# Kernel optimization log

Hardware: AMD Instinct MI355X
Metric: run time of the kernel (lower is better)

## Reference

```python
import jax, jax.numpy as jnp
import numpy as np

N, D, L = 524288, 64, 20  # tokens, in_features, chain depth (20 Linear layers per branch)


def setup_inputs() -> dict:
    key = jax.random.key(0)
    kx, kw, kb = jax.random.split(key, 3)
    x = jax.random.normal(kx, (N, D), dtype=jnp.float32)
    # torch.nn.Linear default init: U(-1/sqrt(fan_in), 1/sqrt(fan_in))
    bound = 1.0 / np.sqrt(D)
    W = jax.random.uniform(kw, (L, D, D), dtype=jnp.float32, minval=-bound, maxval=bound)
    b = jax.random.uniform(kb, (L, D), dtype=jnp.float32, minval=-bound, maxval=bound)
    return {"x": x, "W": W, "b": b}


def reference(x, W, b):
    # is_hit=False => scatter routes ALL tokens to path 1 (path 0 is empty),
    # so forward = branches[1]: 20 sequential Linear(D, D) layers, then a
    # trivial gather (concat of the single non-empty branch result).
    # torch Linear: y = x @ W^T + b, W has shape [out, in].
    def step(h, wb):
        w, bias = wb  # w: [D, D], bias: [D]
        return h @ w.T + bias, None

    out, _ = jax.lax.scan(step, x, (W, b))
    return out
```

## Files before the change

### kernel.cpp

```cpp
#include <hip/hip_runtime.h>
#include <stdint.h>


using short8  = __attribute__((ext_vector_type(8))) short;
using floatx4 = __attribute__((ext_vector_type(4))) float;

#define N_TOK   524288
#define N_LAYER 20
#define FPERM(mt, m) (32 * ((mt) >> 1) + 8 * ((m) >> 2) + 4 * ((mt) & 1) + ((m) & 3))

#ifdef __has_builtin
#if __has_builtin(__builtin_amdgcn_cvt_pk_bf16_f32)
#define HAVE_CVT_PK_BF16 1
#endif
#endif

#ifdef HAVE_CVT_PK_BF16
typedef __bf16 bf16x2_t __attribute__((ext_vector_type(2)));
__device__ __forceinline__ uint32_t pk_bf16(float lo, float hi) {
  union { bf16x2_t v; uint32_t u; } c;
  c.v = __builtin_amdgcn_cvt_pk_bf16_f32(lo, hi);
  return c.u;
}
#else
__device__ __forceinline__ uint32_t pk_bf16(float lo, float hi) {
  uint32_t a = __float_as_uint(lo) + 0x8000u;
  uint32_t b = __float_as_uint(hi) + 0x8000u;
  return __builtin_amdgcn_perm(b, a, 0x07060302u);
}
#endif

__device__ __forceinline__ float upk_lo(uint32_t p) { return __uint_as_float(p << 16); }
__device__ __forceinline__ float upk_hi(uint32_t p) { return __uint_as_float(p & 0xffff0000u); }

__device__ __forceinline__ uint16_t bf16_rne(float f) {
  uint32_t u = __float_as_uint(f);
  u += 0x7fffu + ((u >> 16) & 1u);
  return (uint16_t)(u >> 16);
}
__device__ __forceinline__ float bf16_dec(uint16_t h) {
  return __uint_as_float(((uint32_t)h) << 16);
}

union BFrag { short8 v; uint32_t u[4]; uint4 raw; };
union AFrag { short8 v; uint32_t u[4]; uint4 raw; };

__global__ void prep_split(const float* __restrict__ W,
                           uint16_t* __restrict__ wsh, uint16_t* __restrict__ wsl) {
  int idx  = blockIdx.x * 256 + threadIdx.x;
  int l    = idx >> 9;
  int rem  = idx & 511;
  int frag = rem >> 6;
  int lane = rem & 63;
  int mt = frag >> 1, ks = frag & 1;
  int m  = lane & 15;
  int q  = lane >> 4;
  int wrow = FPERM(mt, m);
  const float* src = W + l * 4096 + wrow * 64 + 32 * ks + 8 * q;
  float4 f0 = *(const float4*)(src);
  float4 f1 = *(const float4*)(src + 4);
  float w[8] = {f0.x, f0.y, f0.z, f0.w, f1.x, f1.y, f1.z, f1.w};
  union { uint16_t s[8]; uint4 v; } oh, ol;
  #pragma unroll
  for (int j = 0; j < 8; j++) {
    uint16_t h = bf16_rne(w[j]);
    oh.s[j] = h;
    ol.s[j] = bf16_rne(w[j] - bf16_dec(h));
  }
  *(uint4*)(wsh + (size_t)idx * 8) = oh.v;
  *(uint4*)(wsl + (size_t)idx * 8) = ol.v;
}

__global__ __launch_bounds__(128, 1) void compose(
    const uint16_t* __restrict__ wsh, const uint16_t* __restrict__ wsl,
    const float* __restrict__ bias,
    uint16_t* __restrict__ afrag, float* __restrict__ vout)
{
  __shared__ float comp[65][64];
  __shared__ __align__(16) float biasLds[N_LAYER * 64];

  const int tid  = threadIdx.x;
  const int twv  = tid >> 6;
  const int lane = tid & 63;
  const int tl   = lane & 15;
  const int q    = lane >> 4;

  for (int i = tid; i < N_LAYER * 64; i += 128) biasLds[i] = bias[i];

  BFrag Bh[4][2], Bl[4][2];
  #pragma unroll
  for (int tb = 0; tb < 4; tb++) {
    const int tok = twv * 64 + tb * 16 + tl;
    #pragma unroll
    for (int ks = 0; ks < 2; ks++)
      #pragma unroll
      for (int p = 0; p < 4; p++) {
        const int f0 = 32 * ks + 8 * q + 2 * p;
        Bh[tb][ks].u[p] = pk_bf16(tok == f0 ? 1.0f : 0.0f, tok == f0 + 1 ? 1.0f : 0.0f);
        Bl[tb][ks].u[p] = 0u;
      }
  }

  const uint4* wph = (const uint4*)wsh;
  const uint4* wpl = (const uint4*)wsl;

  AFrag Ah[8], Al[8];
  #pragma unroll
  for (int f = 0; f < 8; f++) {
    Ah[f].raw = wph[f * 64 + lane];
    Al[f].raw = wpl[f * 64 + lane];
  }

  __syncthreads();

  floatx4 acc[4][4];
  #pragma unroll 2
  for (int l = 0; l < N_LAYER; l++) {
    const int ln = (l + 1 < N_LAYER) ? l + 1 : N_LAYER - 1;
    uint4 nh[8], nl[8];
    #pragma unroll
    for (int f = 0; f < 8; f++) {
      nh[f] = wph[(ln * 8 + f) * 64 + lane];
      nl[f] = wpl[(ln * 8 + f) * 64 + lane];
    }

    #pragma unroll
    for (int mt = 0; mt < 4; mt++) {
      floatx4 bv = *(const floatx4*)(biasLds + l * 64 + 32 * (mt >> 1) + 4 * (mt & 1) + 8 * q);
      #pragma unroll
      for (int tb = 0; tb < 4; tb++) acc[tb][mt] = bv;
    }

    #pragma unroll
    for (int ks = 0; ks < 2; ks++)
      #pragma unroll
      for (int mt = 0; mt < 4; mt++) {
        const int f = mt * 2 + ks;
        #pragma unroll
        for (int tb = 0; tb < 4; tb++) {
          acc[tb][mt] = __builtin_amdgcn_mfma_f32_16x16x32_bf16(Ah[f].v, Bh[tb][ks].v, acc[tb][mt], 0, 0, 0);
          acc[tb][mt] = __builtin_amdgcn_mfma_f32_16x16x32_bf16(Ah[f].v, Bl[tb][ks].v, acc[tb][mt], 0, 0, 0);
          acc[tb][mt] = __builtin_amdgcn_mfma_f32_16x16x32_bf16(Al[f].v, Bh[tb][ks].v, acc[tb][mt], 0, 0, 0);
        }
      }

    if (l == N_LAYER - 1) break;

    #pragma unroll
    for (int tb = 0; tb < 4; tb++)
      #pragma unroll
      for (int mt = 0; mt < 4; mt++) {
        const int ksn = mt >> 1;
        const int d   = 2 * (mt & 1);
        uint32_t u0 = pk_bf16(acc[tb][mt][0], acc[tb][mt][1]);
        uint32_t u1 = pk_bf16(acc[tb][mt][2], acc[tb][mt][3]);
        Bh[tb][ksn].u[d]     = u0;
        Bh[tb][ksn].u[d + 1] = u1;
        Bl[tb][ksn].u[d]     = pk_bf16(acc[tb][mt][0] - upk_lo(u0), acc[tb][mt][1] - upk_hi(u0));
        Bl[tb][ksn].u[d + 1] = pk_bf16(acc[tb][mt][2] - upk_lo(u1), acc[tb][mt][3] - upk_hi(u1));
      }

    #pragma unroll
    for (int f = 0; f < 8; f++) { Ah[f].raw = nh[f]; Al[f].raw = nl[f]; }
  }

  if (twv == 0) {
    #pragma unroll
    for (int tb = 0; tb < 4; tb++)
      #pragma unroll
      for (int mt = 0; mt < 4; mt++)
        *(floatx4*)&comp[tb * 16 + tl][32 * (mt >> 1) + 4 * (mt & 1) + 8 * q] = acc[tb][mt];
  } else if (tl == 0) {
    #pragma unroll
    for (int mt = 0; mt < 4; mt++)
      *(floatx4*)&comp[64][32 * (mt >> 1) + 4 * (mt & 1) + 8 * q] = acc[0][mt];
  }
  __syncthreads();

  for (int it = tid; it < 512; it += 128) {
    const int f  = it >> 6, ln = it & 63;
    const int mt = f >> 1,  ks = f & 1;
    const int m  = ln & 15, qq = ln >> 4;
    const int r  = 16 * mt + m;
    const float vr = comp[64][r];
    union { uint16_t s[8]; uint4 v; } o;
    #pragma unroll
    for (int j = 0; j < 8; j++) o.s[j] = bf16_rne(comp[32 * ks + 8 * qq + j][r] - vr);
    *(uint4*)(afrag + (size_t)it * 8) = o.v;
  }
  if (tid < 64) vout[tid] = comp[64][tid];
}

#define APPLY_BLOCKS 2048

__global__ __launch_bounds__(256, 4) void apply_affine(
    const float* __restrict__ x, const uint16_t* __restrict__ afrag,
    const float* __restrict__ vvec, float* __restrict__ out)
{
  __shared__ __align__(16) uint8_t ldsAll[4][4096];

  const int tid  = threadIdx.x;
  const int wv   = tid >> 6;
  const int lane = tid & 63;
  const int tl   = lane & 15;
  const int q    = lane >> 4;
  uint8_t* lds = ldsAll[wv];

  const uint4* wp = (const uint4*)afrag;
  AFrag Af[8];
  #pragma unroll
  for (int f = 0; f < 8; f++) Af[f].raw = wp[f * 64 + lane];

  floatx4 bv[4];
  #pragma unroll
  for (int mt = 0; mt < 4; mt++)
    bv[mt] = *(const floatx4*)(vvec + 16 * mt + 4 * q);

  for (size_t tokbase = (size_t)blockIdx.x * 128 + (size_t)wv * 32;
       tokbase < (size_t)N_TOK;
       tokbase += (size_t)APPLY_BLOCKS * 128) {

    const float* xp = x + tokbase * 64;
    float4 xr[8];
    #pragma unroll
    for (int j = 0; j < 8; j++)
      xr[j] = *(const float4*)(xp + j * 256 + lane * 4);

    #pragma unroll
    for (int j = 0; j < 8; j++) {
      const uint32_t A = (uint32_t)(j * 512 + lane * 8);
      const uint32_t P = A ^ (((A >> 7) & 7u) << 4);
      uint2 w;
      w.x = pk_bf16(xr[j].x, xr[j].y);
      w.y = pk_bf16(xr[j].z, xr[j].w);
      *(uint2*)(lds + P) = w;
    }

    BFrag Bf[2][2];
    #pragma unroll
    for (int tb = 0; tb < 2; tb++)
      #pragma unroll
      for (int ks = 0; ks < 2; ks++) {
        const uint32_t A = (uint32_t)((tb * 16 + tl) * 128 + ks * 64 + q * 16);
        const uint32_t P = A ^ (((A >> 7) & 7u) << 4);
        Bf[tb][ks].raw = *(const uint4*)(lds + P);
      }

    floatx4 acc[2][4];
    #pragma unroll
    for (int tb = 0; tb < 2; tb++)
      #pragma unroll
      for (int mt = 0; mt < 4; mt++) acc[tb][mt] = bv[mt];

    #pragma unroll
    for (int ks = 0; ks < 2; ks++)
      #pragma unroll
      for (int mt = 0; mt < 4; mt++)
        #pragma unroll
        for (int tb = 0; tb < 2; tb++)
          acc[tb][mt] = __builtin_amdgcn_mfma_f32_16x16x32_bf16(
              Af[mt * 2 + ks].v, Bf[tb][ks].v, acc[tb][mt], 0, 0, 0);

    #pragma unroll
    for (int tb = 0; tb < 2; tb++) {
      #pragma unroll
      for (int mt = 0; mt < 4; mt++) {
        const uint32_t A = (uint32_t)(tl * 256 + mt * 64 + q * 16);
        const uint32_t P = A ^ (((A >> 8) & 7u) << 4);
        *(floatx4*)(lds + P) = acc[tb][mt];
      }
      float* op = out + (tokbase + tb * 16) * 64;
      #pragma unroll
      for (int j = 0; j < 4; j++) {
        const uint32_t A = (uint32_t)(j * 1024 + lane * 16);
        const uint32_t P = A ^ (((A >> 8) & 7u) << 4);
        floatx4 vdat = *(const floatx4*)(lds + P);
        *(floatx4*)(op + j * 256 + lane * 4) = vdat;
      }
    }
  }
}

extern "C" void kernel_launch(void* const* d_in, const int* in_sizes, int n_in,
                              void* d_out, int out_size, void* d_ws, size_t ws_size,
                              hipStream_t stream) {
  (void)in_sizes; (void)n_in; (void)out_size; (void)ws_size;
  const float* x = (const float*)d_in[0];
  const float* W = (const float*)d_in[1];
  const float* b = (const float*)d_in[2];
  float* out = (float*)d_out;

  uint16_t* wsh   = (uint16_t*)d_ws;
  uint16_t* wsl   = (uint16_t*)((char*)d_ws + 163840);
  uint16_t* afrag = (uint16_t*)((char*)d_ws + 327680);
  float*    vvec  = (float*)((char*)d_ws + 335872);

  prep_split<<<dim3(40), dim3(256), 0, stream>>>(W, wsh, wsl);
  compose<<<dim3(1), dim3(128), 0, stream>>>(wsh, wsl, b, afrag, vvec);
  apply_affine<<<dim3(APPLY_BLOCKS), dim3(256), 0, stream>>>(x, afrag, vvec, out);
}
```

Baseline: 273.1 us.

## Stage x directly into LDS via global_load_lds with one tile per wave

The apply kernel drops its grid-stride loop: each wave now handles a single 16-token tile, 8192 blocks are launched and the occupancy hint rises to 6. Input rows are copied straight from global memory into LDS with the global_load_lds builtin using an XOR swizzle, then converted to bf16 from LDS. The bias add moves from the accumulator init to the output store. This aims to cut register pressure and add memory-level parallelism for the bandwidth-bound pass. In exchange each wave reloads the A fragments, and the vmcnt wait serializes the load against compute within a wave.

```diff
diff --git a/kernel.cpp b/kernel.cpp
--- a/kernel.cpp
+++ b/kernel.cpp
@@ -12,6 +12,9 @@
 #ifdef __has_builtin
 #if __has_builtin(__builtin_amdgcn_cvt_pk_bf16_f32)
 #define HAVE_CVT_PK_BF16 1
+#endif
+#if __has_builtin(__builtin_amdgcn_global_load_lds)
+#define HAVE_GLOAD_LDS 1
 #endif
 #endif
 
@@ -191,9 +194,9 @@
   if (tid < 64) vout[tid] = comp[64][tid];
 }
 
-#define APPLY_BLOCKS 2048
-
-__global__ __launch_bounds__(256, 4) void apply_affine(
+#define APPLY_BLOCKS 8192
+
+__global__ __launch_bounds__(256, 6) void apply_affine(
     const float* __restrict__ x, const uint16_t* __restrict__ afrag,
     const float* __restrict__ vvec, float* __restrict__ out)
 {
@@ -206,78 +209,69 @@
   const int q    = lane >> 4;
   uint8_t* lds = ldsAll[wv];
 
+  const size_t tokbase = (size_t)blockIdx.x * 64 + (size_t)wv * 16;
+  const float* xp = x + tokbase * 64;
+
+  #pragma unroll
+  for (int j = 0; j < 4; j++) {
+    const int tok = j * 4 + (lane >> 4);
+    const int g   = (lane & 15) ^ tok;
+    const float* gsrc = xp + tok * 64 + g * 4;
+#ifdef HAVE_GLOAD_LDS
+    __builtin_amdgcn_global_load_lds(
+        (const __attribute__((address_space(1))) uint32_t*)(const void*)gsrc,
+        (__attribute__((address_space(3))) uint32_t*)(void*)(lds + j * 1024),
+        16, 0, 0);
+#else
+    float4 t = *(const float4*)gsrc;
+    *(float4*)(lds + j * 1024 + lane * 16) = t;
+#endif
+  }
+
   const uint4* wp = (const uint4*)afrag;
   AFrag Af[8];
   #pragma unroll
   for (int f = 0; f < 8; f++) Af[f].raw = wp[f * 64 + lane];
-
-  floatx4 bv[4];
-  #pragma unroll
-  for (int mt = 0; mt < 4; mt++)
-    bv[mt] = *(const floatx4*)(vvec + 16 * mt + 4 * q);
-
-  for (size_t tokbase = (size_t)blockIdx.x * 128 + (size_t)wv * 32;
-       tokbase < (size_t)N_TOK;
-       tokbase += (size_t)APPLY_BLOCKS * 128) {
-
-    const float* xp = x + tokbase * 64;
-    float4 xr[8];
-    #pragma unroll
-    for (int j = 0; j < 8; j++)
-      xr[j] = *(const float4*)(xp + j * 256 + lane * 4);
-
-    #pragma unroll
-    for (int j = 0; j < 8; j++) {
-      const uint32_t A = (uint32_t)(j * 512 + lane * 8);
-      const uint32_t P = A ^ (((A >> 7) & 7u) << 4);
-      uint2 w;
-      w.x = pk_bf16(xr[j].x, xr[j].y);
-      w.y = pk_bf16(xr[j].z, xr[j].w);
-      *(uint2*)(lds + P) = w;
-    }
-
-    BFrag Bf[2][2];
-    #pragma unroll
-    for (int tb = 0; tb < 2; tb++)
-      #pragma unroll
-      for (int ks = 0; ks < 2; ks++) {
-        const uint32_t A = (uint32_t)((tb * 16 + tl) * 128 + ks * 64 + q * 16);
-        const uint32_t P = A ^ (((A >> 7) & 7u) << 4);
-        Bf[tb][ks].raw = *(const uint4*)(lds + P);
-      }
-
-    floatx4 acc[2][4];
-    #pragma unroll
-    for (int tb = 0; tb < 2; tb++)
-      #pragma unroll
-      for (int mt = 0; mt < 4; mt++) acc[tb][mt] = bv[mt];
-
-    #pragma unroll
-    for (int ks = 0; ks < 2; ks++)
-      #pragma unroll
-      for (int mt = 0; mt < 4; mt++)
-        #pragma unroll
-        for (int tb = 0; tb < 2; tb++)
-          acc[tb][mt] = __builtin_amdgcn_mfma_f32_16x16x32_bf16(
-              Af[mt * 2 + ks].v, Bf[tb][ks].v, acc[tb][mt], 0, 0, 0);
-
-    #pragma unroll
-    for (int tb = 0; tb < 2; tb++) {
-      #pragma unroll
-      for (int mt = 0; mt < 4; mt++) {
-        const uint32_t A = (uint32_t)(tl * 256 + mt * 64 + q * 16);
-        const uint32_t P = A ^ (((A >> 8) & 7u) << 4);
-        *(floatx4*)(lds + P) = acc[tb][mt];
-      }
-      float* op = out + (tokbase + tb * 16) * 64;
-      #pragma unroll
-      for (int j = 0; j < 4; j++) {
-        const uint32_t A = (uint32_t)(j * 1024 + lane * 16);
-        const uint32_t P = A ^ (((A >> 8) & 7u) << 4);
-        floatx4 vdat = *(const floatx4*)(lds + P);
-        *(floatx4*)(op + j * 256 + lane * 4) = vdat;
-      }
-    }
+  floatx4 vreg = *(const floatx4*)(vvec + tl * 4);
+
+#ifdef HAVE_GLOAD_LDS
+  asm volatile("s_waitcnt vmcnt(0)" ::: "memory");
+#endif
+
+  BFrag Bf[2];
+  #pragma unroll
+  for (int ks = 0; ks < 2; ks++) {
+    floatx4 c0 = *(const floatx4*)(lds + tl * 256 + (((8 * ks + 2 * q + 0) ^ tl) * 16));
+    floatx4 c1 = *(const floatx4*)(lds + tl * 256 + (((8 * ks + 2 * q + 1) ^ tl) * 16));
+    Bf[ks].u[0] = pk_bf16(c0[0], c0[1]);
+    Bf[ks].u[1] = pk_bf16(c0[2], c0[3]);
+    Bf[ks].u[2] = pk_bf16(c1[0], c1[1]);
+    Bf[ks].u[3] = pk_bf16(c1[2], c1[3]);
+  }
+
+  floatx4 acc[4];
+  #pragma unroll
+  for (int mt = 0; mt < 4; mt++) acc[mt] = (floatx4){0.f, 0.f, 0.f, 0.f};
+  #pragma unroll
+  for (int ks = 0; ks < 2; ks++)
+    #pragma unroll
+    for (int mt = 0; mt < 4; mt++)
+      acc[mt] = __builtin_amdgcn_mfma_f32_16x16x32_bf16(
+          Af[mt * 2 + ks].v, Bf[ks].v, acc[mt], 0, 0, 0);
+
+  #pragma unroll
+  for (int mt = 0; mt < 4; mt++) {
+    const uint32_t A = (uint32_t)(tl * 256 + mt * 64 + q * 16);
+    const uint32_t P = A ^ (((A >> 8) & 7u) << 4);
+    *(floatx4*)(lds + P) = acc[mt];
+  }
+  #pragma unroll
+  for (int j = 0; j < 4; j++) {
+    const uint32_t A = (uint32_t)(j * 1024 + lane * 16);
+    const uint32_t P = A ^ (((A >> 8) & 7u) << 4);
+    floatx4 vd = *(const floatx4*)(lds + P);
+    vd[0] += vreg[0]; vd[1] += vreg[1]; vd[2] += vreg[2]; vd[3] += vreg[3];
+    *(floatx4*)(out + (tokbase + j * 4 + (lane >> 4)) * 64 + tl * 4) = vd;
   }
 }
 
```

Result: faster. 262.9 us (-3.7%).
